# Optimization experiments

Measured on AMD Instinct MI355X. Metric: run time of the kernel, lower is better.

## Reference

```python
import jax, jax.numpy as jnp
import numpy as np

B, I, H1, H2, E, T = 16384, 512, 256, 128, 8, 2


def setup_inputs() -> dict:
    key = jax.random.key(0)
    ks = jax.random.split(key, 4)
    # Xavier-ish scaling for stability
    x = jax.random.normal(ks[0], (B, I), dtype=jnp.float32)
    W1 = jax.random.normal(ks[1], (E, I, H1), dtype=jnp.float32) / np.sqrt(I)
    b1 = jnp.zeros((E, H1), dtype=jnp.float32)
    W2 = jax.random.normal(ks[2], (E, H1, H2), dtype=jnp.float32) / np.sqrt(H1)
    b2 = jnp.zeros((E, H2), dtype=jnp.float32)
    Wg = jax.random.normal(ks[3], (T, I, E), dtype=jnp.float32) / np.sqrt(I)
    bg = jnp.zeros((T, E), dtype=jnp.float32)
    return {"x": x, "W1": W1, "b1": b1, "W2": W2, "b2": b2, "Wg": Wg, "bg": bg}


def reference(x, W1, b1, W2, b2, Wg, bg):
    # All experts as one grouped GEMM: [E, B, H1]
    h = jax.nn.relu(jnp.einsum('bi,eih->ebh', x, W1) + b1[:, None, :])
    # Last expert layer (lastlayer_reg=True -> act applied): [E, B, H2]
    e_out = jax.nn.relu(jnp.einsum('ebh,eho->ebo', h, W2) + b2[:, None, :])
    # Per-task gates with softmax over experts: [T, B, E]
    gates = jax.nn.softmax(jnp.einsum('bi,tie->tbe', x, Wg) + bg[:, None, :], axis=-1)
    # Gate-weighted combine of expert outputs: [T, B, H2]
    towers = jnp.einsum('tbe,ebo->tbo', gates, e_out)
    return towers
```

## Files before the change

kernel.cpp:

```cpp
#include <hip/hip_runtime.h>
#include <hip/hip_bf16.h>

#define B_  16384
#define I_  512
#define H1_ 256
#define H2_ 128
#define E_  8
#define T_  2

typedef __attribute__((ext_vector_type(8))) short short8;
typedef __attribute__((ext_vector_type(4))) float float4_t;

__device__ inline unsigned short f2bf(float f) {
    union { float f; unsigned u; } v; v.f = f;
    unsigned r = v.u + 0x7FFFu + ((v.u >> 16) & 1u);
    return (unsigned short)(r >> 16);
}

__device__ inline void async_copy16(const unsigned short* g, unsigned short* l) {
    __builtin_amdgcn_global_load_lds(
        (const __attribute__((address_space(1))) void*)g,
        (__attribute__((address_space(3))) void*)l,
        16, 0, 0);
}

__global__ void transpose_bf16_kernel(const float* __restrict__ in, unsigned short* __restrict__ out,
                                      int R, int C) {
    __shared__ float tile[32][33];
    int e = blockIdx.z;
    int c0 = blockIdx.x * 32;
    int r0 = blockIdx.y * 32;
    const float* inp = in + (size_t)e * R * C;
    unsigned short* outp = out + (size_t)e * R * C;
    int tx = threadIdx.x, ty = threadIdx.y;
#pragma unroll
    for (int j = 0; j < 32; j += 8)
        tile[ty + j][tx] = inp[(size_t)(r0 + ty + j) * C + c0 + tx];
    __syncthreads();
#pragma unroll
    for (int j = 0; j < 32; j += 8)
        outp[(size_t)(c0 + ty + j) * R + r0 + tx] = f2bf(tile[tx][ty + j]);
}

__global__ void prep_wgt_kernel(const float* __restrict__ wg, unsigned short* __restrict__ wgt) {
    int idx = blockIdx.x * 256 + threadIdx.x;
    int te = idx >> 9;
    int i  = idx & 511;
    int t = te >> 3, e = te & 7;
    wgt[(size_t)te * I_ + i] = f2bf(wg[(size_t)t * I_ * E_ + (size_t)i * E_ + e]);
}

__global__ void gates_split_kernel(const float* __restrict__ x,
                                   unsigned short* __restrict__ xb,
                                   const unsigned short* __restrict__ wgt,
                                   const float* __restrict__ bg,
                                   float* __restrict__ gates) {
    __shared__ float red[4][16][16];
    int t = threadIdx.x, w = t >> 6, lane = t & 63;
    int col = lane & 15, quad = lane >> 4;
    int b0 = blockIdx.x * 16;
    int k0 = w * 128;
    const float* xr = x + (size_t)(b0 + col) * I_ + k0 + quad * 8;
    unsigned short* xw = xb + (size_t)(b0 + col) * I_ + k0 + quad * 8;
    const unsigned short* bGp = wgt + (size_t)col * I_ + k0 + quad * 8;
    float4_t acc = {0.f, 0.f, 0.f, 0.f};
#pragma unroll
    for (int ks = 0; ks < 128; ks += 32) {
        float4_t xa = *(const float4_t*)(xr + ks);
        float4_t xc = *(const float4_t*)(xr + ks + 4);
        short8 a;
        a[0] = (short)f2bf(xa[0]); a[1] = (short)f2bf(xa[1]);
        a[2] = (short)f2bf(xa[2]); a[3] = (short)f2bf(xa[3]);
        a[4] = (short)f2bf(xc[0]); a[5] = (short)f2bf(xc[1]);
        a[6] = (short)f2bf(xc[2]); a[7] = (short)f2bf(xc[3]);
        *(short8*)(xw + ks) = a;
        short8 b = *(const short8*)(bGp + ks);
        acc = __builtin_amdgcn_mfma_f32_16x16x32_bf16(a, b, acc, 0, 0, 0);
    }
#pragma unroll
    for (int p = 0; p < 4; ++p)
        red[w][quad * 4 + p][col] = acc[p];
    __syncthreads();
    int r = t >> 4, te = t & 15;
    float v = red[0][r][te] + red[1][r][te] + red[2][r][te] + red[3][r][te] + bg[te];
    float m = v;
    m = fmaxf(m, __shfl_xor(m, 1));
    m = fmaxf(m, __shfl_xor(m, 2));
    m = fmaxf(m, __shfl_xor(m, 4));
    float ev = __expf(v - m);
    float s = ev;
    s += __shfl_xor(s, 1);
    s += __shfl_xor(s, 2);
    s += __shfl_xor(s, 4);
    gates[(size_t)te * B_ + b0 + r] = ev / s;
}

__global__ void gemm_relu_kernel(const unsigned short* __restrict__ A, size_t aSE,
                                 const unsigned short* __restrict__ Bt, size_t bSE,
                                 const float* __restrict__ bias, int biasSE,
                                 unsigned short* __restrict__ C, size_t cSE,
                                 int K, int lda, int ldb, int ldc) {
    __shared__ unsigned short smem[128 * 128];
    unsigned short* As = smem;
    unsigned short* Bs = smem + 128 * 64;
    int e = blockIdx.z;
    const unsigned short* Ae = A + (size_t)e * aSE;
    const unsigned short* Be = Bt + (size_t)e * bSE;
    const float* biasE = bias + (size_t)e * biasSE;
    unsigned short* Ce = C + (size_t)e * cSE;
    int m0 = blockIdx.x * 128, n0 = blockIdx.y * 128;
    int t = threadIdx.x, w = t >> 6, lane = t & 63;
    int col = lane & 15, quad = lane >> 4;
    int wm = (w & 1) * 64, wn = (w >> 1) * 64;

    float4_t acc[4][4];
#pragma unroll
    for (int mi = 0; mi < 4; ++mi)
#pragma unroll
        for (int ni = 0; ni < 4; ++ni)
            acc[mi][ni] = (float4_t){0.f, 0.f, 0.f, 0.f};

    int rT = t >> 3;
    int gk = (((t & 7) ^ (rT & 7))) * 8;
    const unsigned short* aG = Ae + (size_t)(m0 + rT) * lda + gk;
    const unsigned short* bG = Be + (size_t)(n0 + rT) * ldb + gk;
    unsigned short* aL = As + (size_t)w * 64 * 8;
    unsigned short* bL = Bs + (size_t)w * 64 * 8;

    for (int k0 = 0; k0 < K; k0 += 64) {
#pragma unroll
        for (int j = 0; j < 4; ++j) {
            async_copy16(aG + (size_t)j * 32 * lda + k0, aL + j * 2048);
            async_copy16(bG + (size_t)j * 32 * ldb + k0, bL + j * 2048);
        }
        __syncthreads();
#pragma unroll
        for (int kk = 0; kk < 64; kk += 32) {
            int q = (kk >> 3) + quad;
            short8 af[4], bf[4];
#pragma unroll
            for (int mi = 0; mi < 4; ++mi) {
                int r = wm + mi * 16 + col;
                af[mi] = *(const short8*)&As[r * 64 + ((q ^ (r & 7)) * 8)];
            }
#pragma unroll
            for (int ni = 0; ni < 4; ++ni) {
                int r = wn + ni * 16 + col;
                bf[ni] = *(const short8*)&Bs[r * 64 + ((q ^ (r & 7)) * 8)];
            }
#pragma unroll
            for (int mi = 0; mi < 4; ++mi)
#pragma unroll
                for (int ni = 0; ni < 4; ++ni)
                    acc[mi][ni] = __builtin_amdgcn_mfma_f32_16x16x32_bf16(af[mi], bf[ni], acc[mi][ni], 0, 0, 0);
        }
        __syncthreads();
    }
    unsigned short* Ct = smem;
#pragma unroll
    for (int ni = 0; ni < 4; ++ni) {
        int c = wn + ni * 16 + col;
        float bv = biasE[n0 + c];
#pragma unroll
        for (int mi = 0; mi < 4; ++mi) {
            int rbase = wm + mi * 16 + quad * 4;
#pragma unroll
            for (int p = 0; p < 4; ++p) {
                float v = acc[mi][ni][p] + bv;
                v = v > 0.f ? v : 0.f;
                Ct[(rbase + p) * 128 + c] = f2bf(v);
            }
        }
    }
    __syncthreads();
    int rr = t >> 4, sl = t & 15;
#pragma unroll
    for (int pass = 0; pass < 8; ++pass) {
        int row = pass * 16 + rr;
        short8 vv = *(const short8*)&Ct[row * 128 + sl * 8];
        *(short8*)&Ce[(size_t)(m0 + row) * ldc + n0 + sl * 8] = vv;
    }
}

__global__ void fused_l2_combine_kernel(const unsigned short* __restrict__ h,
                                        const unsigned short* __restrict__ w2t,
                                        const float* __restrict__ b2,
                                        const float* __restrict__ gates,
                                        float* __restrict__ out) {
    __shared__ unsigned short As[32 * 128];
    __shared__ unsigned short Bs[64 * 128];
    __shared__ float gL[16 * 32];

    int b0 = blockIdx.x * 32;
    int nh = blockIdx.y * 64;
    int t = threadIdx.x, w = t >> 6, lane = t & 63;
    int col = lane & 15, quad = lane >> 4;
    int wn = w * 16;

    if (t < 128) {
        int te = t >> 3, i4 = (t & 7) * 4;
        *(float4_t*)&gL[te * 32 + i4] = *(const float4_t*)&gates[(size_t)te * B_ + b0 + i4];
    }

    float4_t tw0[2], tw1[2];
#pragma unroll
    for (int mi = 0; mi < 2; ++mi) {
        tw0[mi] = (float4_t){0.f, 0.f, 0.f, 0.f};
        tw1[mi] = (float4_t){0.f, 0.f, 0.f, 0.f};
    }

    int rT = t >> 4;
    int slot = t & 15;

    for (int e = 0; e < E_; ++e) {
        const unsigned short* hE = h + (size_t)e * B_ * H1_;
        const unsigned short* w2E = w2t + (size_t)e * H2_ * H1_ + (size_t)nh * H1_;

        float4_t acc[2];
#pragma unroll
        for (int mi = 0; mi < 2; ++mi)
            acc[mi] = (float4_t){0.f, 0.f, 0.f, 0.f};

        for (int k0 = 0; k0 < H1_; k0 += 128) {
#pragma unroll
            for (int j = 0; j < 2; ++j) {
                int row = j * 16 + rT;
                int gk = (((slot ^ row) & 7) | (slot & 8)) * 8;
                async_copy16(hE + (size_t)(b0 + row) * H1_ + k0 + gk,
                             As + j * 2048 + w * 512);
            }
#pragma unroll
            for (int j = 0; j < 4; ++j) {
                int row = j * 16 + rT;
                int gk = (((slot ^ row) & 7) | (slot & 8)) * 8;
                async_copy16(w2E + (size_t)row * H1_ + k0 + gk,
                             Bs + j * 2048 + w * 512);
            }
            __syncthreads();
#pragma unroll
            for (int kk = 0; kk < 128; kk += 32) {
                int q = (kk >> 3) + quad;
                short8 af[2], bfr;
#pragma unroll
                for (int mi = 0; mi < 2; ++mi) {
                    int r = mi * 16 + col;
                    int sw = ((q & 8) | ((q ^ r) & 7)) * 8;
                    af[mi] = *(const short8*)&As[r * 128 + sw];
                }
                {
                    int r = wn + col;
                    int sw = ((q & 8) | ((q ^ r) & 7)) * 8;
                    bfr = *(const short8*)&Bs[r * 128 + sw];
                }
#pragma unroll
                for (int mi = 0; mi < 2; ++mi)
                    acc[mi] = __builtin_amdgcn_mfma_f32_16x16x32_bf16(af[mi], bfr, acc[mi], 0, 0, 0);
            }
            __syncthreads();
        }

        float bv = b2[e * H2_ + nh + wn + col];
#pragma unroll
        for (int mi = 0; mi < 2; ++mi) {
            float4_t g0 = *(const float4_t*)&gL[e * 32 + mi * 16 + quad * 4];
            float4_t g1 = *(const float4_t*)&gL[(8 + e) * 32 + mi * 16 + quad * 4];
#pragma unroll
            for (int p = 0; p < 4; ++p) {
                float v = acc[mi][p] + bv;
                v = v > 0.f ? v : 0.f;
                tw0[mi][p] += g0[p] * v;
                tw1[mi][p] += g1[p] * v;
            }
        }
    }

    int n = nh + wn + col;
#pragma unroll
    for (int mi = 0; mi < 2; ++mi) {
#pragma unroll
        for (int p = 0; p < 4; ++p) {
            int r = b0 + mi * 16 + quad * 4 + p;
            out[(size_t)r * H2_ + n] = tw0[mi][p];
            out[(size_t)B_ * H2_ + (size_t)r * H2_ + n] = tw1[mi][p];
        }
    }
}

extern "C" void kernel_launch(void* const* d_in, const int* in_sizes, int n_in,
                              void* d_out, int out_size, void* d_ws, size_t ws_size,
                              hipStream_t stream) {
    const float* x  = (const float*)d_in[0];
    const float* W1 = (const float*)d_in[1];
    const float* b1 = (const float*)d_in[2];
    const float* W2 = (const float*)d_in[3];
    const float* b2 = (const float*)d_in[4];
    const float* Wg = (const float*)d_in[5];
    const float* bg = (const float*)d_in[6];
    float* out = (float*)d_out;

    char* ws = (char*)d_ws;
    unsigned short* xb    = (unsigned short*)(ws);
    unsigned short* w1t   = (unsigned short*)(ws + 16777216);
    unsigned short* w2t   = (unsigned short*)(ws + 18874368);
    unsigned short* wgt   = (unsigned short*)(ws + 19398656);
    float*          gates = (float*)(ws + 19415040);
    unsigned short* h     = (unsigned short*)(ws + 20463616);

    transpose_bf16_kernel<<<dim3(H1_ / 32, I_ / 32, E_), dim3(32, 8), 0, stream>>>(W1, w1t, I_, H1_);
    transpose_bf16_kernel<<<dim3(H2_ / 32, H1_ / 32, E_), dim3(32, 8), 0, stream>>>(W2, w2t, H1_, H2_);
    prep_wgt_kernel<<<dim3(T_ * E_ * I_ / 256), 256, 0, stream>>>(Wg, wgt);

    gates_split_kernel<<<dim3(B_ / 16), 256, 0, stream>>>(x, xb, wgt, bg, gates);

    gemm_relu_kernel<<<dim3(B_ / 128, H1_ / 128, E_), 256, 0, stream>>>(
        xb, 0, w1t, (size_t)H1_ * I_, b1, H1_, h, (size_t)B_ * H1_, I_, I_, I_, H1_);

    fused_l2_combine_kernel<<<dim3(B_ / 32, 2), 256, 0, stream>>>(h, w2t, b2, gates, out);
}
```

Baseline: 165.1 us.

## Merge prep kernels into one launch, pad epilogue LDS, retile layer-2 combine

The two weight transposes, the gate-weight prep and the gates computation now run as a single kernel dispatched by block index. Each gates block transposes Wg into LDS itself instead of reading a prepared global copy, which removes three launches and one workspace buffer. The gemm epilogue staging buffer gets a 136-element row stride to avoid LDS bank conflicts. The layer-2 combine kernel drops LDS staging and async copies: each block handles 16 rows and all 128 outputs, loading MFMA fragments directly from global memory. The risks are redundant Wg conversion in every gates block and uncoalesced, unreused global fragment loads in the combine kernel.

```diff
diff --git a/kernel.cpp b/kernel.cpp
--- a/kernel.cpp
+++ b/kernel.cpp
@@ -24,75 +24,94 @@
         16, 0, 0);
 }
 
-__global__ void transpose_bf16_kernel(const float* __restrict__ in, unsigned short* __restrict__ out,
-                                      int R, int C) {
-    __shared__ float tile[32][33];
-    int e = blockIdx.z;
-    int c0 = blockIdx.x * 32;
-    int r0 = blockIdx.y * 32;
-    const float* inp = in + (size_t)e * R * C;
-    unsigned short* outp = out + (size_t)e * R * C;
-    int tx = threadIdx.x, ty = threadIdx.y;
-#pragma unroll
-    for (int j = 0; j < 32; j += 8)
-        tile[ty + j][tx] = inp[(size_t)(r0 + ty + j) * C + c0 + tx];
-    __syncthreads();
-#pragma unroll
-    for (int j = 0; j < 32; j += 8)
-        outp[(size_t)(c0 + ty + j) * R + r0 + tx] = f2bf(tile[tx][ty + j]);
-}
-
-__global__ void prep_wgt_kernel(const float* __restrict__ wg, unsigned short* __restrict__ wgt) {
-    int idx = blockIdx.x * 256 + threadIdx.x;
-    int te = idx >> 9;
-    int i  = idx & 511;
-    int t = te >> 3, e = te & 7;
-    wgt[(size_t)te * I_ + i] = f2bf(wg[(size_t)t * I_ * E_ + (size_t)i * E_ + e]);
-}
-
-__global__ void gates_split_kernel(const float* __restrict__ x,
-                                   unsigned short* __restrict__ xb,
-                                   const unsigned short* __restrict__ wgt,
-                                   const float* __restrict__ bg,
-                                   float* __restrict__ gates) {
-    __shared__ float red[4][16][16];
-    int t = threadIdx.x, w = t >> 6, lane = t & 63;
-    int col = lane & 15, quad = lane >> 4;
-    int b0 = blockIdx.x * 16;
-    int k0 = w * 128;
-    const float* xr = x + (size_t)(b0 + col) * I_ + k0 + quad * 8;
-    unsigned short* xw = xb + (size_t)(b0 + col) * I_ + k0 + quad * 8;
-    const unsigned short* bGp = wgt + (size_t)col * I_ + k0 + quad * 8;
-    float4_t acc = {0.f, 0.f, 0.f, 0.f};
-#pragma unroll
-    for (int ks = 0; ks < 128; ks += 32) {
-        float4_t xa = *(const float4_t*)(xr + ks);
-        float4_t xc = *(const float4_t*)(xr + ks + 4);
-        short8 a;
-        a[0] = (short)f2bf(xa[0]); a[1] = (short)f2bf(xa[1]);
-        a[2] = (short)f2bf(xa[2]); a[3] = (short)f2bf(xa[3]);
-        a[4] = (short)f2bf(xc[0]); a[5] = (short)f2bf(xc[1]);
-        a[6] = (short)f2bf(xc[2]); a[7] = (short)f2bf(xc[3]);
-        *(short8*)(xw + ks) = a;
-        short8 b = *(const short8*)(bGp + ks);
-        acc = __builtin_amdgcn_mfma_f32_16x16x32_bf16(a, b, acc, 0, 0, 0);
-    }
-#pragma unroll
-    for (int p = 0; p < 4; ++p)
-        red[w][quad * 4 + p][col] = acc[p];
-    __syncthreads();
-    int r = t >> 4, te = t & 15;
-    float v = red[0][r][te] + red[1][r][te] + red[2][r][te] + red[3][r][te] + bg[te];
-    float m = v;
-    m = fmaxf(m, __shfl_xor(m, 1));
-    m = fmaxf(m, __shfl_xor(m, 2));
-    m = fmaxf(m, __shfl_xor(m, 4));
-    float ev = __expf(v - m);
-    float s = ev;
-    s += __shfl_xor(s, 1);
-    s += __shfl_xor(s, 2);
-    s += __shfl_xor(s, 4);
-    gates[(size_t)te * B_ + b0 + r] = ev / s;
+__global__ void prep_gates_kernel(const float* __restrict__ x,
+                                  unsigned short* __restrict__ xb,
+                                  const float* __restrict__ W1,
+                                  unsigned short* __restrict__ w1t,
+                                  const float* __restrict__ W2,
+                                  unsigned short* __restrict__ w2t,
+                                  const float* __restrict__ Wg,
+                                  const float* __restrict__ bg,
+                                  float* __restrict__ gates) {
+    __shared__ __align__(16) char smem[16 * 520 * 2 + 4 * 16 * 16 * 4];
+    int bid = blockIdx.x;
+    int t = threadIdx.x;
+
+    if (bid < 1024) {
+        unsigned short* wgtL = (unsigned short*)smem;
+        float (*red)[16][16] = (float (*)[16][16])(smem + 16 * 520 * 2);
+#pragma unroll
+        for (int j = 0; j < 32; ++j) {
+            int idx = j * 256 + t;
+            int e = idx & 7, i = (idx >> 3) & 511, task = idx >> 12;
+            wgtL[(task * 8 + e) * 520 + i] = f2bf(Wg[idx]);
+        }
+        __syncthreads();
+
+        int w = t >> 6, lane = t & 63;
+        int col = lane & 15, quad = lane >> 4;
+        int b0 = bid * 16;
+        int k0 = w * 128;
+        const float* xr = x + (size_t)(b0 + col) * I_ + k0 + quad * 8;
+        unsigned short* xw = xb + (size_t)(b0 + col) * I_ + k0 + quad * 8;
+        const unsigned short* bL = &wgtL[col * 520 + k0 + quad * 8];
+        float4_t acc = {0.f, 0.f, 0.f, 0.f};
+#pragma unroll
+        for (int ks = 0; ks < 128; ks += 32) {
+            float4_t xa = *(const float4_t*)(xr + ks);
+            float4_t xc = *(const float4_t*)(xr + ks + 4);
+            short8 a;
+            a[0] = (short)f2bf(xa[0]); a[1] = (short)f2bf(xa[1]);
+            a[2] = (short)f2bf(xa[2]); a[3] = (short)f2bf(xa[3]);
+            a[4] = (short)f2bf(xc[0]); a[5] = (short)f2bf(xc[1]);
+            a[6] = (short)f2bf(xc[2]); a[7] = (short)f2bf(xc[3]);
+            *(short8*)(xw + ks) = a;
+            short8 b = *(const short8*)(bL + ks);
+            acc = __builtin_amdgcn_mfma_f32_16x16x32_bf16(a, b, acc, 0, 0, 0);
+        }
+#pragma unroll
+        for (int p = 0; p < 4; ++p)
+            red[w][quad * 4 + p][col] = acc[p];
+        __syncthreads();
+        int r = t >> 4, te = t & 15;
+        float v = red[0][r][te] + red[1][r][te] + red[2][r][te] + red[3][r][te] + bg[te];
+        float m = v;
+        m = fmaxf(m, __shfl_xor(m, 1));
+        m = fmaxf(m, __shfl_xor(m, 2));
+        m = fmaxf(m, __shfl_xor(m, 4));
+        float ev = __expf(v - m);
+        float s = ev;
+        s += __shfl_xor(s, 1);
+        s += __shfl_xor(s, 2);
+        s += __shfl_xor(s, 4);
+        gates[(size_t)te * B_ + b0 + r] = ev / s;
+    } else {
+        float (*tile)[33] = (float (*)[33])smem;
+        const float* in; unsigned short* outp; int R, C, e, r0, c0;
+        if (bid < 2048) {
+            int tl = bid - 1024;
+            e = tl >> 7; int rem = tl & 127;
+            R = I_; C = H1_;
+            r0 = (rem >> 3) * 32; c0 = (rem & 7) * 32;
+            in = W1; outp = w1t;
+        } else {
+            int tl = bid - 2048;
+            e = tl >> 5; int rem = tl & 31;
+            R = H1_; C = H2_;
+            r0 = (rem >> 2) * 32; c0 = (rem & 3) * 32;
+            in = W2; outp = w2t;
+        }
+        const float* inp = in + (size_t)e * R * C;
+        unsigned short* op = outp + (size_t)e * R * C;
+        int tx = t & 31, ty = t >> 5;
+#pragma unroll
+        for (int j = 0; j < 32; j += 8)
+            tile[ty + j][tx] = inp[(size_t)(r0 + ty + j) * C + c0 + tx];
+        __syncthreads();
+#pragma unroll
+        for (int j = 0; j < 32; j += 8)
+            op[(size_t)(c0 + ty + j) * R + r0 + tx] = f2bf(tile[tx][ty + j]);
+    }
 }
 
 __global__ void gemm_relu_kernel(const unsigned short* __restrict__ A, size_t aSE,
@@ -100,7 +119,7 @@
                                  const float* __restrict__ bias, int biasSE,
                                  unsigned short* __restrict__ C, size_t cSE,
                                  int K, int lda, int ldb, int ldc) {
-    __shared__ unsigned short smem[128 * 128];
+    __shared__ unsigned short smem[128 * 136];
     unsigned short* As = smem;
     unsigned short* Bs = smem + 128 * 64;
     int e = blockIdx.z;
@@ -168,7 +187,7 @@
             for (int p = 0; p < 4; ++p) {
                 float v = acc[mi][ni][p] + bv;
                 v = v > 0.f ? v : 0.f;
-                Ct[(rbase + p) * 128 + c] = f2bf(v);
+                Ct[(rbase + p) * 136 + c] = f2bf(v);
             }
         }
     }
@@ -177,7 +196,7 @@
 #pragma unroll
     for (int pass = 0; pass < 8; ++pass) {
         int row = pass * 16 + rr;
-        short8 vv = *(const short8*)&Ct[row * 128 + sl * 8];
+        short8 vv = *(const short8*)&Ct[row * 136 + sl * 8];
         *(short8*)&Ce[(size_t)(m0 + row) * ldc + n0 + sl * 8] = vv;
     }
 }
@@ -187,101 +206,64 @@
                                         const float* __restrict__ b2,
                                         const float* __restrict__ gates,
                                         float* __restrict__ out) {
-    __shared__ unsigned short As[32 * 128];
-    __shared__ unsigned short Bs[64 * 128];
-    __shared__ float gL[16 * 32];
-
-    int b0 = blockIdx.x * 32;
-    int nh = blockIdx.y * 64;
+    __shared__ float gL[16][16];
+    int b0 = blockIdx.x * 16;
     int t = threadIdx.x, w = t >> 6, lane = t & 63;
     int col = lane & 15, quad = lane >> 4;
-    int wn = w * 16;
-
-    if (t < 128) {
-        int te = t >> 3, i4 = (t & 7) * 4;
-        *(float4_t*)&gL[te * 32 + i4] = *(const float4_t*)&gates[(size_t)te * B_ + b0 + i4];
-    }
+    int wn = w * 32;
+
+    {
+        int te = t >> 4, r = t & 15;
+        gL[te][r] = gates[(size_t)te * B_ + b0 + r];
+    }
+    __syncthreads();
 
     float4_t tw0[2], tw1[2];
 #pragma unroll
-    for (int mi = 0; mi < 2; ++mi) {
-        tw0[mi] = (float4_t){0.f, 0.f, 0.f, 0.f};
-        tw1[mi] = (float4_t){0.f, 0.f, 0.f, 0.f};
-    }
-
-    int rT = t >> 4;
-    int slot = t & 15;
+    for (int nt = 0; nt < 2; ++nt) {
+        tw0[nt] = (float4_t){0.f, 0.f, 0.f, 0.f};
+        tw1[nt] = (float4_t){0.f, 0.f, 0.f, 0.f};
+    }
+
+    const unsigned short* hRow = h + (size_t)(b0 + col) * H1_ + quad * 8;
 
     for (int e = 0; e < E_; ++e) {
-        const unsigned short* hE = h + (size_t)e * B_ * H1_;
-        const unsigned short* w2E = w2t + (size_t)e * H2_ * H1_ + (size_t)nh * H1_;
+        const unsigned short* hE = hRow + (size_t)e * B_ * H1_;
+        const unsigned short* w2E = w2t + ((size_t)e * H2_ + wn + col) * H1_ + quad * 8;
 
         float4_t acc[2];
-#pragma unroll
-        for (int mi = 0; mi < 2; ++mi)
-            acc[mi] = (float4_t){0.f, 0.f, 0.f, 0.f};
-
-        for (int k0 = 0; k0 < H1_; k0 += 128) {
-#pragma unroll
-            for (int j = 0; j < 2; ++j) {
-                int row = j * 16 + rT;
-                int gk = (((slot ^ row) & 7) | (slot & 8)) * 8;
-                async_copy16(hE + (size_t)(b0 + row) * H1_ + k0 + gk,
-                             As + j * 2048 + w * 512);
-            }
-#pragma unroll
-            for (int j = 0; j < 4; ++j) {
-                int row = j * 16 + rT;
-                int gk = (((slot ^ row) & 7) | (slot & 8)) * 8;
-                async_copy16(w2E + (size_t)row * H1_ + k0 + gk,
-                             Bs + j * 2048 + w * 512);
-            }
-            __syncthreads();
-#pragma unroll
-            for (int kk = 0; kk < 128; kk += 32) {
-                int q = (kk >> 3) + quad;
-                short8 af[2], bfr;
-#pragma unroll
-                for (int mi = 0; mi < 2; ++mi) {
-                    int r = mi * 16 + col;
-                    int sw = ((q & 8) | ((q ^ r) & 7)) * 8;
-                    af[mi] = *(const short8*)&As[r * 128 + sw];
-                }
-                {
-                    int r = wn + col;
-                    int sw = ((q & 8) | ((q ^ r) & 7)) * 8;
-                    bfr = *(const short8*)&Bs[r * 128 + sw];
-                }
-#pragma unroll
-                for (int mi = 0; mi < 2; ++mi)
-                    acc[mi] = __builtin_amdgcn_mfma_f32_16x16x32_bf16(af[mi], bfr, acc[mi], 0, 0, 0);
-            }
-            __syncthreads();
-        }
-
-        float bv = b2[e * H2_ + nh + wn + col];
-#pragma unroll
-        for (int mi = 0; mi < 2; ++mi) {
-            float4_t g0 = *(const float4_t*)&gL[e * 32 + mi * 16 + quad * 4];
-            float4_t g1 = *(const float4_t*)&gL[(8 + e) * 32 + mi * 16 + quad * 4];
-#pragma unroll
-            for (int p = 0; p < 4; ++p) {
-                float v = acc[mi][p] + bv;
-                v = v > 0.f ? v : 0.f;
-                tw0[mi][p] += g0[p] * v;
-                tw1[mi][p] += g1[p] * v;
-            }
-        }
-    }
-
-    int n = nh + wn + col;
-#pragma unroll
-    for (int mi = 0; mi < 2; ++mi) {
+        acc[0] = (float4_t){0.f, 0.f, 0.f, 0.f};
+        acc[1] = (float4_t){0.f, 0.f, 0.f, 0.f};
+#pragma unroll
+        for (int kk = 0; kk < H1_; kk += 32) {
+            short8 a  = *(const short8*)(hE + kk);
+            short8 f0 = *(const short8*)(w2E + kk);
+            short8 f1 = *(const short8*)(w2E + (size_t)16 * H1_ + kk);
+            acc[0] = __builtin_amdgcn_mfma_f32_16x16x32_bf16(a, f0, acc[0], 0, 0, 0);
+            acc[1] = __builtin_amdgcn_mfma_f32_16x16x32_bf16(a, f1, acc[1], 0, 0, 0);
+        }
+
+        float bv0 = b2[e * H2_ + wn + col];
+        float bv1 = b2[e * H2_ + wn + 16 + col];
 #pragma unroll
         for (int p = 0; p < 4; ++p) {
-            int r = b0 + mi * 16 + quad * 4 + p;
-            out[(size_t)r * H2_ + n] = tw0[mi][p];
-            out[(size_t)B_ * H2_ + (size_t)r * H2_ + n] = tw1[mi][p];
+            int r = quad * 4 + p;
+            float g0 = gL[e][r], g1 = gL[8 + e][r];
+            float v0 = acc[0][p] + bv0; v0 = v0 > 0.f ? v0 : 0.f;
+            float v1 = acc[1][p] + bv1; v1 = v1 > 0.f ? v1 : 0.f;
+            tw0[0][p] += g0 * v0;  tw0[1][p] += g0 * v1;
+            tw1[0][p] += g1 * v0;  tw1[1][p] += g1 * v1;
+        }
+    }
+
+#pragma unroll
+    for (int nt = 0; nt < 2; ++nt) {
+        int n = wn + nt * 16 + col;
+#pragma unroll
+        for (int p = 0; p < 4; ++p) {
+            int r = b0 + quad * 4 + p;
+            out[(size_t)r * H2_ + n] = tw0[nt][p];
+            out[(size_t)B_ * H2_ + (size_t)r * H2_ + n] = tw1[nt][p];
         }
     }
 }
@@ -302,18 +284,13 @@
     unsigned short* xb    = (unsigned short*)(ws);
     unsigned short* w1t   = (unsigned short*)(ws + 16777216);
     unsigned short* w2t   = (unsigned short*)(ws + 18874368);
-    unsigned short* wgt   = (unsigned short*)(ws + 19398656);
-    float*          gates = (float*)(ws + 19415040);
-    unsigned short* h     = (unsigned short*)(ws + 20463616);
-
-    transpose_bf16_kernel<<<dim3(H1_ / 32, I_ / 32, E_), dim3(32, 8), 0, stream>>>(W1, w1t, I_, H1_);
-    transpose_bf16_kernel<<<dim3(H2_ / 32, H1_ / 32, E_), dim3(32, 8), 0, stream>>>(W2, w2t, H1_, H2_);
-    prep_wgt_kernel<<<dim3(T_ * E_ * I_ / 256), 256, 0, stream>>>(Wg, wgt);
-
-    gates_split_kernel<<<dim3(B_ / 16), 256, 0, stream>>>(x, xb, wgt, bg, gates);
+    float*          gates = (float*)(ws + 19398656);
+    unsigned short* h     = (unsigned short*)(ws + 20447232);
+
+    prep_gates_kernel<<<dim3(2304), 256, 0, stream>>>(x, xb, W1, w1t, W2, w2t, Wg, bg, gates);
 
     gemm_relu_kernel<<<dim3(B_ / 128, H1_ / 128, E_), 256, 0, stream>>>(
         xb, 0, w1t, (size_t)H1_ * I_, b1, H1_, h, (size_t)B_ * H1_, I_, I_, I_, H1_);
 
-    fused_l2_combine_kernel<<<dim3(B_ / 32, 2), 256, 0, stream>>>(h, w2t, b2, gates, out);
-}
+    fused_l2_combine_kernel<<<dim3(B_ / 16), 256, 0, stream>>>(h, w2t, b2, gates, out);
+}
```

New measurement: 226.2 us. 37.0% more time.
